# Performance work log

Measured on AMD Instinct MI355X. Metric: run time of the kernel, lower is better.

## Reference

```python
import jax, jax.numpy as jnp
import numpy as np
import math

B, S, D, H = 64, 575, 256, 8
FF = 4 * D
EPS = 1e-5
DILATIONS = (1, 2, 4)


def _ln(x, g, b):
    mu = jnp.mean(x, axis=-1, keepdims=True)
    var = jnp.var(x, axis=-1, keepdims=True)
    return (x - mu) * jax.lax.rsqrt(var + EPS) * g + b


def setup_inputs() -> dict:
    key = jax.random.key(0)
    ks = jax.random.split(key, 8)
    w = lambda k, shape: jax.random.normal(k, shape, jnp.float32) * 0.02
    return {
        'state': jax.random.normal(ks[0], (B, S, D), jnp.float32),
        'conv_w': w(ks[1], (3, D, D, 3, 3)),
        'conv_b': jnp.zeros((3, D), jnp.float32),
        'qkv_w': w(ks[2], (3 * D, D)),
        'qkv_b': jnp.zeros((3 * D,), jnp.float32),
        'o_w': w(ks[3], (D, D)),
        'o_b': jnp.zeros((D,), jnp.float32),
        'attn_bias': w(ks[4], (H, S, S)),
        'ffp_w': w(ks[5], (FF, D)),
        'ffp_b': jnp.zeros((FF,), jnp.float32),
        'ffg_w': w(ks[6], (FF, D)),
        'ffg_b': jnp.zeros((FF,), jnp.float32),
        'ffo_w': w(ks[7], (D, FF)),
        'ffo_b': jnp.zeros((D,), jnp.float32),
        'n1_g': jnp.ones((D,), jnp.float32), 'n1_b': jnp.zeros((D,), jnp.float32),
        'n2_g': jnp.ones((D,), jnp.float32), 'n2_b': jnp.zeros((D,), jnp.float32),
        'n3_g': jnp.ones((D,), jnp.float32), 'n3_b': jnp.zeros((D,), jnp.float32),
    }


def _forward(state, conv_w, conv_b, qkv_w, qkv_b, o_w, o_b, attn_bias,
             ffp_w, ffp_b, ffg_w, ffg_b, ffo_w, ffo_b,
             n1_g, n1_b, n2_g, n2_b, n3_g, n3_b):
    b, s, d = state.shape
    h = attn_bias.shape[0]
    hd = d // h
    spatial = int(round(math.sqrt(s + 1)))  # grid_size + 1; spatial^2 == s+1 here

    # --- multi-scale dilated conv mixing ---
    pad = jnp.zeros((b, 1, d), state.dtype)
    h2d = jnp.concatenate([pad, state], axis=1)            # (B, S+1, D)
    h2d = jnp.transpose(h2d, (0, 2, 1)).reshape(b, d, spatial, spatial)
    conv_sum = 0.0
    for i, dil in enumerate(DILATIONS):
        y = jax.lax.conv_general_dilated(
            h2d, conv_w[i], window_strides=(1, 1),
            padding=[(dil, dil), (dil, dil)], rhs_dilation=(dil, dil),
            dimension_numbers=('NCHW', 'OIHW', 'NCHW'))
        conv_sum = conv_sum + y + conv_b[i][None, :, None, None]
    h_flat = jnp.transpose(conv_sum.reshape(b, d, -1), (0, 2, 1))  # (B, S+1, D)
    hmix = h_flat[:, 1:, :]

    state = _ln(state + hmix, n1_g, n1_b)

    # --- self-attention with learned per-head pair bias ---
    qkv = state @ qkv_w.T + qkv_b                          # (B, S, 3D)
    q, k, v = jnp.split(qkv, 3, axis=-1)
    # NOTE: replicate torch's reshape (no transpose): (B,S,D) -> (B,H,S,hd)
    q = q.reshape(b, h, s, hd)
    k = k.reshape(b, h, s, hd)
    v = v.reshape(b, h, s, hd)
    scores = jnp.einsum('bhsd,bhtd->bhst', q, k) / math.sqrt(hd)
    scores = scores + attn_bias[None]
    attn = jax.nn.softmax(scores, axis=-1)
    out = jnp.einsum('bhst,bhtd->bhsd', attn, v)
    out = jnp.transpose(out, (0, 2, 1, 3)).reshape(b, s, d)

    state = _ln(state + out @ o_w.T + o_b, n2_g, n2_b)

    # --- gated feed-forward ---
    proj = state @ ffp_w.T + ffp_b
    gate = jax.nn.sigmoid(state @ ffg_w.T + ffg_b)
    ff = (proj * gate) @ ffo_w.T + ffo_b
    return _ln(state + ff, n3_g, n3_b)


def reference(state, conv_w, conv_b, qkv_w, qkv_b, o_w, o_b, attn_bias,
              ffp_w, ffp_b, ffg_w, ffg_b, ffo_w, ffo_b,
              n1_g, n1_b, n2_g, n2_b, n3_g, n3_b):
    return _forward(state, conv_w, conv_b, qkv_w, qkv_b, o_w, o_b, attn_bias,
                    ffp_w, ffp_b, ffg_w, ffg_b, ffo_w, ffo_b,
                    n1_g, n1_b, n2_g, n2_b, n3_g, n3_b)
```

## Files before the change

### kernel.cpp

```cpp
#include <hip/hip_runtime.h>
#include <hip/hip_bf16.h>
#include <cstdio>


typedef __attribute__((ext_vector_type(8))) short s8v;
typedef __attribute__((ext_vector_type(4))) float f32x4;
typedef unsigned short u16;

constexpr int kB = 64, kS = 575, kD = 256, kH = 8, kP = 576, kFF = 1024;
constexpr int kRows = kB * kS;
constexpr float kEps = 1e-5f;
constexpr float kScale = 0.17677669529663687f;
constexpr size_t kPdStride = 9420800;

__device__ __forceinline__ u16 f2b(float f) {
  __hip_bfloat16 h = __float2bfloat16(f);
  return *reinterpret_cast<u16*>(&h);
}
__device__ __forceinline__ void unpack2(unsigned int w, float& lo, float& hi) {
  union { float f; unsigned int u; } a, b;
  a.u = w << 16;
  b.u = w & 0xffff0000u;
  lo = a.f;
  hi = b.f;
}

__device__ __forceinline__ void gll16(const void* g, void* l) {
  __builtin_amdgcn_global_load_lds((const __attribute__((address_space(1))) void*)g,
                                   (__attribute__((address_space(3))) void*)l, 16, 0, 0);
}

__global__ void k_pack_convw(const float* __restrict__ cw, u16* __restrict__ wc) {
  const int blk = blockIdx.x;
  const int ci = threadIdx.x;
  const int i = blk >> 8, co = blk & 255;
  const float* src = cw + (size_t)blk * 2304 + ci * 9;
  float v[9];
#pragma unroll
  for (int r = 0; r < 9; ++r) v[r] = src[r];
#pragma unroll
  for (int r = 0; r < 9; ++r)
    wc[(((size_t)(i * 9 + r)) << 16) + (co << 8) + ci] = f2b(v[r]);
}

__global__ void k_tobf16(const float* __restrict__ in, u16* __restrict__ out, int n) {
  int i = blockIdx.x * 256 + threadIdx.x;
  if (i < n) out[i] = f2b(in[i]);
}

__global__ void k_make_x0(const float* __restrict__ state, u16* __restrict__ x0,
                          u16* __restrict__ zrow) {
  int bp = blockIdx.x;
  int c = threadIdx.x;
  if (bp == kB * kP) { zrow[c] = 0; return; }
  int p = bp % kP;
  int b = bp / kP;
  float v = (p == 0) ? 0.f : state[((size_t)(b * kS + p - 1)) * kD + c];
  x0[(size_t)bp * kD + c] = f2b(v);
}

__global__ __launch_bounds__(256) void k_gemm(const u16* __restrict__ A,
                                              const u16* __restrict__ Bw,
                                              const float* __restrict__ bias,
                                              u16* __restrict__ Cb,
                                              int M, int N, int K) {
  __shared__ u16 As[2][8192];
  __shared__ u16 Bs[2][8192];
  const int t = threadIdx.x;
  const int wave = t >> 6, lane = t & 63;
  const int wm = wave >> 1, wn = wave & 1;
  const int lr = lane & 15, lk = lane >> 4;
  const int m0 = blockIdx.x * 128, n0 = blockIdx.y * 128;
  const int lrow = lane >> 3;
  const int swzk = ((lane & 7) ^ lrow) * 8;
  const u16 *ga[4], *gb[4];
#pragma unroll
  for (int i = 0; i < 4; ++i) {
    int r = 8 * wave + lrow + 32 * i;
    int ra = m0 + r;
    if (ra > M - 1) ra = M - 1;
    ga[i] = A + (size_t)ra * K + swzk;
    gb[i] = Bw + (size_t)(n0 + r) * K + swzk;
  }
  auto stage = [&](int kt, int buf) {
#pragma unroll
    for (int i = 0; i < 4; ++i) {
      gll16(ga[i] + kt, &As[buf][i * 2048 + wave * 512]);
      gll16(gb[i] + kt, &Bs[buf][i * 2048 + wave * 512]);
    }
  };
  f32x4 acc[4][4] = {};
  stage(0, 0);
  __syncthreads();
  const int NT = K >> 6;
  for (int s = 0; s < NT; ++s) {
    const int cur = s & 1;
    if (s + 1 < NT) stage((s + 1) << 6, cur ^ 1);
    s8v af[2][4], bfr[2][4];
#pragma unroll
    for (int kk = 0; kk < 2; ++kk)
#pragma unroll
      for (int i = 0; i < 4; ++i) {
        const int rA = wm * 64 + i * 16 + lr;
        const int rB = wn * 64 + i * 16 + lr;
        af[kk][i] = *(const s8v*)(&As[cur][rA * 64 + ((kk * 32 + lk * 8) ^ ((rA & 7) << 3))]);
        bfr[kk][i] = *(const s8v*)(&Bs[cur][rB * 64 + ((kk * 32 + lk * 8) ^ ((rB & 7) << 3))]);
      }
#pragma unroll
    for (int kk = 0; kk < 2; ++kk)
#pragma unroll
      for (int i = 0; i < 4; ++i)
#pragma unroll
        for (int j = 0; j < 4; ++j)
          acc[i][j] = __builtin_amdgcn_mfma_f32_16x16x32_bf16(af[kk][i], bfr[kk][j], acc[i][j], 0, 0, 0);
    __syncthreads();
  }
#pragma unroll
  for (int i = 0; i < 4; ++i) {
    const int rbase = m0 + wm * 64 + i * 16 + lk * 4;
#pragma unroll
    for (int j = 0; j < 4; ++j) {
      const int col = n0 + wn * 64 + j * 16 + lr;
      const float bv = bias[col];
#pragma unroll
      for (int q = 0; q < 4; ++q) {
        int r = rbase + q;
        if (r < M) Cb[(size_t)r * N + col] = f2b(acc[i][j][q] + bv);
      }
    }
  }
}

__global__ __launch_bounds__(256) void k_ff1(const u16* __restrict__ A,
                                             const u16* __restrict__ Wf,
                                             const float* __restrict__ pb,
                                             const float* __restrict__ gb,
                                             u16* __restrict__ H, int M) {
  __shared__ u16 As[2][4096];
  __shared__ u16 Bp[2][4096];
  __shared__ u16 Bg[2][4096];
  const int t = threadIdx.x;
  const int wave = t >> 6;
  const int wm = wave >> 1, wn = wave & 1;
  const int lr = t & 15, lk = (t & 63) >> 4;
  const int m0 = blockIdx.x * 128, n0 = blockIdx.y * 128;
  int ra = m0 + (t >> 2);
  int rb = ra + 64;
  if (ra > M - 1) ra = M - 1;
  if (rb > M - 1) rb = M - 1;
  const int koff = (((t & 3) ^ ((t >> 2) & 3)) * 8);
  const u16* gA0 = A + (size_t)ra * kD + koff;
  const u16* gA1 = A + (size_t)rb * kD + koff;
  const u16* gP0 = Wf + (size_t)(n0 + (t >> 2)) * kD + koff;
  const u16* gP1 = gP0 + (size_t)64 * kD;
  const u16* gG0 = gP0 + (size_t)1024 * kD;
  const u16* gG1 = gP1 + (size_t)1024 * kD;
  auto stage = [&](int kt, int buf) {
    gll16(gA0 + kt, &As[buf][wave * 512]);
    gll16(gA1 + kt, &As[buf][2048 + wave * 512]);
    gll16(gP0 + kt, &Bp[buf][wave * 512]);
    gll16(gP1 + kt, &Bp[buf][2048 + wave * 512]);
    gll16(gG0 + kt, &Bg[buf][wave * 512]);
    gll16(gG1 + kt, &Bg[buf][2048 + wave * 512]);
  };
  f32x4 ap[4][4] = {};
  f32x4 ag[4][4] = {};
  stage(0, 0);
  __syncthreads();
  for (int s = 0; s < 8; ++s) {
    const int cur = s & 1;
    if (s < 7) stage((s + 1) << 5, cur ^ 1);
    s8v af[4], bp4[4], bg4[4];
#pragma unroll
    for (int i = 0; i < 4; ++i) {
      const int rA = wm * 64 + i * 16 + lr;
      const int rB = wn * 64 + i * 16 + lr;
      const int oA = rA * 32 + ((lk * 8) ^ ((rA & 3) << 3));
      const int oB = rB * 32 + ((lk * 8) ^ ((rB & 3) << 3));
      af[i] = *(const s8v*)(&As[cur][oA]);
      bp4[i] = *(const s8v*)(&Bp[cur][oB]);
      bg4[i] = *(const s8v*)(&Bg[cur][oB]);
    }
#pragma unroll
    for (int i = 0; i < 4; ++i)
#pragma unroll
      for (int j = 0; j < 4; ++j) {
        ap[i][j] = __builtin_amdgcn_mfma_f32_16x16x32_bf16(af[i], bp4[j], ap[i][j], 0, 0, 0);
        ag[i][j] = __builtin_amdgcn_mfma_f32_16x16x32_bf16(af[i], bg4[j], ag[i][j], 0, 0, 0);
      }
    __syncthreads();
  }
#pragma unroll
  for (int i = 0; i < 4; ++i) {
    const int rbase = m0 + wm * 64 + i * 16 + lk * 4;
#pragma unroll
    for (int j = 0; j < 4; ++j) {
      const int col = n0 + wn * 64 + j * 16 + lr;
      const float pbv = pb[col], gbv = gb[col];
#pragma unroll
      for (int q = 0; q < 4; ++q) {
        int r = rbase + q;
        if (r < M) {
          float p = ap[i][j][q] + pbv;
          float g = ag[i][j][q] + gbv;
          H[(size_t)r * kFF + col] = f2b(p * (1.f / (1.f + __expf(-g))));
        }
      }
    }
  }
}

__global__ __launch_bounds__(256) void k_conv(const u16* __restrict__ X0,
                                              const u16* __restrict__ zrow,
                                              const u16* __restrict__ Wc,
                                              const float* __restrict__ cb,
                                              u16* __restrict__ pd) {
  __shared__ u16 As[2][8192];
  __shared__ u16 Bs[2][8192];
  const int t = threadIdx.x;
  const int wave = t >> 6, lane = t & 63;
  const int wm = wave >> 1, wn = wave & 1;
  const int lr = lane & 15, lk = lane >> 4;
  const int m0 = blockIdx.x * 128;
  const int n0 = blockIdx.y * 128;
  const int di = blockIdx.z;
  const int dil = 1 << di;
  const int lrow = lane >> 3;
  const int swzk = ((lane & 7) ^ lrow) * 8;
  const u16* Wd = Wc + ((size_t)di * 9 << 16);
  int py[4], px[4];
  const u16* xrow[4];
  const u16* gw[4];
#pragma unroll
  for (int i = 0; i < 4; ++i) {
    int r = 8 * wave + lrow + 32 * i;
    int m = m0 + r;
    int bbv = m / 576;
    int p = m - bbv * 576;
    py[i] = p / 24;
    px[i] = p - py[i] * 24;
    xrow[i] = X0 + (((size_t)(bbv * kP)) << 8) + swzk;
    gw[i] = Wd + (size_t)(n0 + r) * kD + swzk;
  }
  const u16* S0[4];
  const u16* S1[4];
  auto csrc = [&](const u16** dst, int dyv, int dxv) {
#pragma unroll
    for (int i = 0; i < 4; ++i) {
      const int ny = py[i] + dyv, nx = px[i] + dxv;
      const bool v = ((unsigned)ny < 24u) & ((unsigned)nx < 24u);
      dst[i] = v ? xrow[i] + ((ny * 24 + nx) << 8) : zrow + swzk;
    }
  };
  auto stage = [&](const u16* const* S, size_t woff, int kc, int buf) {
#pragma unroll
    for (int i = 0; i < 4; ++i) {
      gll16(S[i] + kc, &As[buf][i * 2048 + wave * 512]);
      gll16(gw[i] + woff + kc, &Bs[buf][i * 2048 + wave * 512]);
    }
  };
  f32x4 acc[4][4] = {};
  csrc(S0, -dil, -dil);
  stage(S0, 0, 0, 0);
  stage(S0, 0, 64, 1);
  for (int tap = 0; tap < 9; ++tap) {
    if (tap < 8) {
      const int tn = tap + 1;
      csrc(S1, (tn / 3 - 1) * dil, (tn % 3 - 1) * dil);
    }
    const size_t woff = (size_t)tap << 16;
#pragma unroll
    for (int c = 0; c < 4; ++c) {
      const int buf = c & 1;
      if (c == 3 && tap == 8) {
        asm volatile("s_waitcnt vmcnt(0)" ::: "memory");
      } else {
        asm volatile("s_waitcnt vmcnt(8)" ::: "memory");
      }
      __builtin_amdgcn_s_barrier();
      s8v af[2][4], bfr[2][4];
#pragma unroll
      for (int kk = 0; kk < 2; ++kk)
#pragma unroll
        for (int ii = 0; ii < 4; ++ii) {
          const int rA = wm * 64 + ii * 16 + lr;
          const int rB = wn * 64 + ii * 16 + lr;
          af[kk][ii] = *(const s8v*)(&As[buf][rA * 64 + ((kk * 32 + lk * 8) ^ ((rA & 7) << 3))]);
          bfr[kk][ii] = *(const s8v*)(&Bs[buf][rB * 64 + ((kk * 32 + lk * 8) ^ ((rB & 7) << 3))]);
        }
#pragma unroll
      for (int kk = 0; kk < 2; ++kk)
#pragma unroll
        for (int ii = 0; ii < 4; ++ii)
#pragma unroll
          for (int jj = 0; jj < 4; ++jj)
            acc[ii][jj] = __builtin_amdgcn_mfma_f32_16x16x32_bf16(af[kk][ii], bfr[kk][jj], acc[ii][jj], 0, 0, 0);
      __builtin_amdgcn_s_barrier();
      if (c == 0) {
        stage(S0, woff, 128, buf);
      } else if (c == 1) {
        stage(S0, woff, 192, buf);
      } else if (c == 2) {
        if (tap < 8) stage(S1, woff + 65536, 0, buf);
      } else {
        if (tap < 8) stage(S1, woff + 65536, 64, buf);
      }
    }
#pragma unroll
    for (int i = 0; i < 4; ++i) S0[i] = S1[i];
  }
  u16* pdo = pd + (size_t)di * kPdStride;
#pragma unroll
  for (int i2 = 0; i2 < 4; ++i2) {
    const int mbase = m0 + wm * 64 + i2 * 16 + lk * 4;
#pragma unroll
    for (int j = 0; j < 4; ++j) {
      const int col = n0 + wn * 64 + j * 16 + lr;
      const float bv = cb[di * kD + col];
#pragma unroll
      for (int q = 0; q < 4; ++q) {
        const int m = mbase + q;
        const int b2 = m / 576;
        const int p = m - b2 * 576;
        if (p >= 1)
          pdo[((size_t)(b2 * kS + p - 1) << 8) + col] = f2b(acc[i2][j][q] + bv);
      }
    }
  }
}

__global__ __launch_bounds__(256) void k_attn2(const u16* __restrict__ qkv,
                                               const float* __restrict__ bias,
                                               u16* __restrict__ outp) {
  __shared__ u16 KsS[2][2048];
  __shared__ u16 VtS[2][2048];
  __shared__ u16 PsS[4][1024];
  const int qt = blockIdx.x, h = blockIdx.y, b = blockIdx.z;
  const int tid = threadIdx.x;
  const int w = tid >> 6, lane = tid & 63;
  const int lg = lane >> 4, lr = lane & 15;
  const int q0 = qt * 64;
  const int qrow_a = q0 + w * 16 + lr;
  const int qrow_ac = qrow_a < kS ? qrow_a : kS - 1;
  s8v qf;
  {
    int F = h * (kS * 32) + qrow_ac * 32 + lg * 8;
    qf = *(const s8v*)(qkv + ((size_t)(b * kS + (F >> 8))) * 768 + (F & 255));
  }
  const int trel = tid >> 2;
  const int dcol = (tid & 3) * 8;
  float mrun[4], lsum[4];
#pragma unroll
  for (int r = 0; r < 4; ++r) { mrun[r] = -1e30f; lsum[r] = 0.f; }
  f32x4 o0 = {0.f, 0.f, 0.f, 0.f}, o1 = {0.f, 0.f, 0.f, 0.f};
  const f32x4 zf = {0.f, 0.f, 0.f, 0.f};
  const int qrow_s = q0 + w * 16 + lg * 4;
  const size_t kvrowbase = (size_t)(b * kS) * 768;

  for (int kt = 0; kt < 9; ++kt) {
    const int t0 = kt * 64;
    const int buf = kt & 1;
    {
      const int tg = t0 + trel;
      const bool tv = tg < kS;
      const int tcl = tv ? tg : kS - 1;
      const int Fk = h * (kS * 32) + tcl * 32 + dcol;
      const u16* kp = qkv + kvrowbase + (size_t)(Fk >> 8) * 768 + 256 + (Fk & 255);
      uint4 kd = {0, 0, 0, 0}, vd = {0, 0, 0, 0};
      if (tv) {
        kd = *(const uint4*)kp;
        vd = *(const uint4*)(kp + 256);
      }
      *(uint4*)&KsS[buf][trel * 32 + (dcol ^ ((trel & 3) << 3))] = kd;
      union { uint4 u4; u16 us[8]; } vu;
      vu.u4 = vd;
#pragma unroll
      for (int j = 0; j < 8; ++j) {
        const int d = dcol + j;
        VtS[buf][d * 64 + (trel ^ ((d & 7) << 3))] = vu.us[j];
      }
    }
    float bv[4][4];
#pragma unroll
    for (int r = 0; r < 4; ++r) {
      const int qr = qrow_s + r;
      const float* bp = bias + ((size_t)h * kS + (qr < kS ? qr : kS - 1)) * kS;
#pragma unroll
      for (int j = 0; j < 4; ++j) {
        const int tg = t0 + j * 16 + lr;
        bv[j][r] = (tg < kS) ? bp[tg] : -1e30f;
      }
    }
    __syncthreads();
    f32x4 sc[4];
#pragma unroll
    for (int j = 0; j < 4; ++j) {
      const int krow = j * 16 + lr;
      s8v kf = *(const s8v*)&KsS[buf][krow * 32 + ((lg * 8) ^ ((krow & 3) << 3))];
      sc[j] = __builtin_amdgcn_mfma_f32_16x16x32_bf16(qf, kf, zf, 0, 0, 0);
    }
#pragma unroll
    for (int r = 0; r < 4; ++r) {
      float s4[4];
      float sm = -1e30f;
#pragma unroll
      for (int j = 0; j < 4; ++j) {
        s4[j] = fmaf(sc[j][r], kScale, bv[j][r]);
        sm = fmaxf(sm, s4[j]);
      }
      sm = fmaxf(sm, __shfl_xor(sm, 1));
      sm = fmaxf(sm, __shfl_xor(sm, 2));
      sm = fmaxf(sm, __shfl_xor(sm, 4));
      sm = fmaxf(sm, __shfl_xor(sm, 8));
      const float nm = fmaxf(mrun[r], sm);
      const float corr = __expf(mrun[r] - nm);
      mrun[r] = nm;
      float psum = 0.f;
      const int prow = lg * 4 + r;
#pragma unroll
      for (int j = 0; j < 4; ++j) {
        const float p = __expf(s4[j] - nm);
        psum += p;
        PsS[w][prow * 64 + ((j * 16 + lr) ^ ((prow & 7) << 3))] = f2b(p);
      }
      lsum[r] = fmaf(lsum[r], corr, psum);
      o0[r] *= corr;
      o1[r] *= corr;
    }
#pragma unroll
    for (int c = 0; c < 2; ++c) {
      const int pcol = c * 32 + lg * 8;
      s8v pf = *(const s8v*)&PsS[w][lr * 64 + (pcol ^ ((lr & 7) << 3))];
      s8v vf0 = *(const s8v*)&VtS[buf][lr * 64 + (pcol ^ ((lr & 7) << 3))];
      s8v vf1 = *(const s8v*)&VtS[buf][(16 + lr) * 64 + (pcol ^ (((16 + lr) & 7) << 3))];
      o0 = __builtin_amdgcn_mfma_f32_16x16x32_bf16(pf, vf0, o0, 0, 0, 0);
      o1 = __builtin_amdgcn_mfma_f32_16x16x32_bf16(pf, vf1, o1, 0, 0, 0);
    }
  }
#pragma unroll
  for (int r = 0; r < 4; ++r) {
    float lt = lsum[r];
    lt += __shfl_xor(lt, 1);
    lt += __shfl_xor(lt, 2);
    lt += __shfl_xor(lt, 4);
    lt += __shfl_xor(lt, 8);
    const float inv = 1.f / lt;
    const int qr = qrow_s + r;
    if (qr < kS) {
      u16* op = outp + ((size_t)(b * kS + qr)) * kD + h * 32;
      op[lr] = f2b(o0[r] * inv);
      op[16 + lr] = f2b(o1[r] * inv);
    }
  }
}

__global__ __launch_bounds__(256) void k_add_ln(const float* __restrict__ xa,
                                                const u16* __restrict__ xb,
                                                const float* __restrict__ g,
                                                const float* __restrict__ be,
                                                float* __restrict__ of, u16* __restrict__ ob) {
  const int wave = threadIdx.x >> 6, lane = threadIdx.x & 63;
  const int row = blockIdx.x * 4 + wave;
  const float4 a = ((const float4*)(xa + (size_t)row * kD))[lane];
  uint2 bw = ((const uint2*)(xb + (size_t)row * kD))[lane];
  float b0, b1, b2, b3;
  unpack2(bw.x, b0, b1);
  unpack2(bw.y, b2, b3);
  float x0 = a.x + b0, x1 = a.y + b1, x2 = a.z + b2, x3 = a.w + b3;
  float sum = x0 + x1 + x2 + x3;
  float sq = fmaf(x0, x0, fmaf(x1, x1, fmaf(x2, x2, x3 * x3)));
  for (int off = 1; off < 64; off <<= 1) {
    sum += __shfl_xor(sum, off);
    sq += __shfl_xor(sq, off);
  }
  const float mean = sum * (1.f / 256.f);
  const float var = sq * (1.f / 256.f) - mean * mean;
  const float rs = rsqrtf(var + kEps);
  const float4 gg = ((const float4*)g)[lane];
  const float4 bt = ((const float4*)be)[lane];
  float y0 = (x0 - mean) * rs * gg.x + bt.x;
  float y1 = (x1 - mean) * rs * gg.y + bt.y;
  float y2 = (x2 - mean) * rs * gg.z + bt.z;
  float y3 = (x3 - mean) * rs * gg.w + bt.w;
  float4 yo = {y0, y1, y2, y3};
  ((float4*)(of + (size_t)row * kD))[lane] = yo;
  if (ob) {
    u16* po = ob + (size_t)row * kD + lane * 4;
    po[0] = f2b(y0); po[1] = f2b(y1); po[2] = f2b(y2); po[3] = f2b(y3);
  }
}

__global__ __launch_bounds__(256) void k_add_ln3(const float* __restrict__ xa,
                                                 const u16* __restrict__ pa,
                                                 const u16* __restrict__ pbq,
                                                 const u16* __restrict__ pc,
                                                 const float* __restrict__ g,
                                                 const float* __restrict__ be,
                                                 float* __restrict__ of, u16* __restrict__ ob) {
  const int wave = threadIdx.x >> 6, lane = threadIdx.x & 63;
  const int row = blockIdx.x * 4 + wave;
  const size_t base = (size_t)row * kD;
  const float4 a = ((const float4*)(xa + base))[lane];
  uint2 w0 = ((const uint2*)(pa + base))[lane];
  uint2 w1 = ((const uint2*)(pbq + base))[lane];
  uint2 w2 = ((const uint2*)(pc + base))[lane];
  float a0, a1, a2, a3, c0, c1, c2, c3, d0, d1, d2, d3;
  unpack2(w0.x, a0, a1); unpack2(w0.y, a2, a3);
  unpack2(w1.x, c0, c1); unpack2(w1.y, c2, c3);
  unpack2(w2.x, d0, d1); unpack2(w2.y, d2, d3);
  float x0 = a.x + a0 + c0 + d0, x1 = a.y + a1 + c1 + d1;
  float x2 = a.z + a2 + c2 + d2, x3 = a.w + a3 + c3 + d3;
  float sum = x0 + x1 + x2 + x3;
  float sq = fmaf(x0, x0, fmaf(x1, x1, fmaf(x2, x2, x3 * x3)));
  for (int off = 1; off < 64; off <<= 1) {
    sum += __shfl_xor(sum, off);
    sq += __shfl_xor(sq, off);
  }
  const float mean = sum * (1.f / 256.f);
  const float var = sq * (1.f / 256.f) - mean * mean;
  const float rs = rsqrtf(var + kEps);
  const float4 gg = ((const float4*)g)[lane];
  const float4 bt = ((const float4*)be)[lane];
  float y0 = (x0 - mean) * rs * gg.x + bt.x;
  float y1 = (x1 - mean) * rs * gg.y + bt.y;
  float y2 = (x2 - mean) * rs * gg.z + bt.z;
  float y3 = (x3 - mean) * rs * gg.w + bt.w;
  float4 yo = {y0, y1, y2, y3};
  ((float4*)(of + base))[lane] = yo;
  u16* po = ob + base + lane * 4;
  po[0] = f2b(y0); po[1] = f2b(y1); po[2] = f2b(y2); po[3] = f2b(y3);
}

extern "C" void kernel_launch(void* const* d_in, const int* in_sizes, int n_in,
                              void* d_out, int out_size, void* d_ws, size_t ws_size,
                              hipStream_t stream) {
  const float* state = (const float*)d_in[0];
  const float* conv_w = (const float*)d_in[1];
  const float* conv_b = (const float*)d_in[2];
  const float* qkv_w = (const float*)d_in[3];
  const float* qkv_b = (const float*)d_in[4];
  const float* o_w = (const float*)d_in[5];
  const float* o_b = (const float*)d_in[6];
  const float* attn_bias = (const float*)d_in[7];
  const float* ffp_w = (const float*)d_in[8];
  const float* ffp_b = (const float*)d_in[9];
  const float* ffg_w = (const float*)d_in[10];
  const float* ffg_b = (const float*)d_in[11];
  const float* ffo_w = (const float*)d_in[12];
  const float* ffo_b = (const float*)d_in[13];
  const float* n1_g = (const float*)d_in[14];
  const float* n1_b = (const float*)d_in[15];
  const float* n2_g = (const float*)d_in[16];
  const float* n2_b = (const float*)d_in[17];
  const float* n3_g = (const float*)d_in[18];
  const float* n3_b = (const float*)d_in[19];

  constexpr size_t kWsNeed = 137527296;
  if (ws_size < kWsNeed) {
    fprintf(stderr, "[kernel] ws_size=%zu < need=%zu\n", ws_size, kWsNeed);
    return;
  }
  char* ws = (char*)d_ws;
  u16* Wc = (u16*)(ws + 0);
  u16* Wqkv = (u16*)(ws + 3538944);
  u16* Wo = (u16*)(ws + 3932160);
  u16* Wff = (u16*)(ws + 4063232);
  u16* Wffo = (u16*)(ws + 5111808);
  float* stF = (float*)(ws + 5636096);
  u16* stB = (u16*)(ws + 43319296);
  char* S4 = ws + 62160896;
  u16* X0 = (u16*)(ws + 5636096);
  u16* zrow = (u16*)(ws + 43319296);
  u16* pd = (u16*)S4;
  u16* qkvb = (u16*)S4;
  u16* attnout = (u16*)(S4 + 56524800);
  u16* oprojb = (u16*)S4;
  u16* ffh = (u16*)S4;
  float* outp = (float*)d_out;

  k_pack_convw<<<768, 256, 0, stream>>>(conv_w, Wc);
  k_tobf16<<<768, 256, 0, stream>>>(qkv_w, Wqkv, 768 * 256);
  k_tobf16<<<256, 256, 0, stream>>>(o_w, Wo, 256 * 256);
  k_tobf16<<<1024, 256, 0, stream>>>(ffp_w, Wff, 1024 * 256);
  k_tobf16<<<1024, 256, 0, stream>>>(ffg_w, Wff + 1024 * 256, 1024 * 256);
  k_tobf16<<<1024, 256, 0, stream>>>(ffo_w, Wffo, 256 * 1024);
  k_make_x0<<<kB * kP + 1, 256, 0, stream>>>(state, X0, zrow);

  k_conv<<<dim3(288, 2, 3), 256, 0, stream>>>(X0, zrow, Wc, conv_b, pd);
  k_add_ln3<<<kRows / 4, 256, 0, stream>>>(state, pd, pd + kPdStride, pd + 2 * kPdStride,
                                           n1_g, n1_b, stF, stB);

  k_gemm<<<dim3(288, 6), 256, 0, stream>>>(stB, Wqkv, qkv_b, qkvb, kRows, 768, 256);
  k_attn2<<<dim3(9, kH, kB), 256, 0, stream>>>(qkvb, attn_bias, attnout);
  k_gemm<<<dim3(288, 2), 256, 0, stream>>>(attnout, Wo, o_b, oprojb, kRows, 256, 256);
  k_add_ln<<<kRows / 4, 256, 0, stream>>>(stF, oprojb, n2_g, n2_b, stF, stB);

  k_ff1<<<dim3(288, 8), 256, 0, stream>>>(stB, Wff, ffp_b, ffg_b, ffh, kRows);
  k_gemm<<<dim3(288, 2), 256, 0, stream>>>(ffh, Wffo, ffo_b, stB, kRows, 256, 1024);
  k_add_ln<<<kRows / 4, 256, 0, stream>>>(stF, stB, n3_g, n3_b, outp, nullptr);
}
```

Baseline: 516.9 us.

## Make GEMMs persistent over multiple M tiles with cross-tile prefetch pipeline

Each GEMM block now processes several consecutive 128-row M tiles, flattening tile and K iterations into one loop. The next stage's loads are issued across tile boundaries, so the prologue and epilogue latency of each tile is hidden. Explicit vmcnt waits and raw barriers replace __syncthreads to keep two stages in flight. The trade-off is fewer blocks, which lowers occupancy and parallelism; the hand-counted vmcnt values depend on the exact number of loads issued per stage.

```diff
diff --git a/kernel.cpp b/kernel.cpp
--- a/kernel.cpp
+++ b/kernel.cpp
@@ -63,39 +63,48 @@
                                               const u16* __restrict__ Bw,
                                               const float* __restrict__ bias,
                                               u16* __restrict__ Cb,
-                                              int M, int N, int K) {
+                                              int M, int N, int K, int MT, int ntSh) {
   __shared__ u16 As[2][8192];
   __shared__ u16 Bs[2][8192];
   const int t = threadIdx.x;
   const int wave = t >> 6, lane = t & 63;
   const int wm = wave >> 1, wn = wave & 1;
   const int lr = lane & 15, lk = lane >> 4;
-  const int m0 = blockIdx.x * 128, n0 = blockIdx.y * 128;
+  const int n0 = blockIdx.y * 128;
   const int lrow = lane >> 3;
   const int swzk = ((lane & 7) ^ lrow) * 8;
-  const u16 *ga[4], *gb[4];
+  int roff[4];
+  const u16* gb[4];
 #pragma unroll
   for (int i = 0; i < 4; ++i) {
     int r = 8 * wave + lrow + 32 * i;
-    int ra = m0 + r;
-    if (ra > M - 1) ra = M - 1;
-    ga[i] = A + (size_t)ra * K + swzk;
+    roff[i] = r;
     gb[i] = Bw + (size_t)(n0 + r) * K + swzk;
   }
-  auto stage = [&](int kt, int buf) {
+  const int NT = 1 << ntSh;
+  const int U = MT << ntSh;
+  auto stage = [&](int u, int buf) {
+    const int mt = u >> ntSh;
+    const int kt = (u & (NT - 1)) << 6;
+    const int m0 = (blockIdx.x * MT + mt) << 7;
 #pragma unroll
     for (int i = 0; i < 4; ++i) {
-      gll16(ga[i] + kt, &As[buf][i * 2048 + wave * 512]);
+      int ra = m0 + roff[i];
+      if (ra > M - 1) ra = M - 1;
+      gll16(A + (size_t)ra * K + kt + swzk, &As[buf][i * 2048 + wave * 512]);
       gll16(gb[i] + kt, &Bs[buf][i * 2048 + wave * 512]);
     }
   };
   f32x4 acc[4][4] = {};
   stage(0, 0);
-  __syncthreads();
-  const int NT = K >> 6;
-  for (int s = 0; s < NT; ++s) {
-    const int cur = s & 1;
-    if (s + 1 < NT) stage((s + 1) << 6, cur ^ 1);
+  if (U > 1) stage(1, 1);
+  for (int u = 0; u < U; ++u) {
+    const int cur = u & 1;
+    if (u + 1 < U)
+      asm volatile("s_waitcnt vmcnt(8)" ::: "memory");
+    else
+      asm volatile("s_waitcnt vmcnt(0)" ::: "memory");
+    __builtin_amdgcn_s_barrier();
     s8v af[2][4], bfr[2][4];
 #pragma unroll
     for (int kk = 0; kk < 2; ++kk)
@@ -113,19 +122,24 @@
 #pragma unroll
         for (int j = 0; j < 4; ++j)
           acc[i][j] = __builtin_amdgcn_mfma_f32_16x16x32_bf16(af[kk][i], bfr[kk][j], acc[i][j], 0, 0, 0);
-    __syncthreads();
-  }
-#pragma unroll
-  for (int i = 0; i < 4; ++i) {
-    const int rbase = m0 + wm * 64 + i * 16 + lk * 4;
-#pragma unroll
-    for (int j = 0; j < 4; ++j) {
-      const int col = n0 + wn * 64 + j * 16 + lr;
-      const float bv = bias[col];
-#pragma unroll
-      for (int q = 0; q < 4; ++q) {
-        int r = rbase + q;
-        if (r < M) Cb[(size_t)r * N + col] = f2b(acc[i][j][q] + bv);
+    __builtin_amdgcn_s_barrier();
+    if (u + 2 < U) stage(u + 2, cur);
+    if ((u & (NT - 1)) == NT - 1) {
+      const int m0 = (blockIdx.x * MT + (u >> ntSh)) << 7;
+#pragma unroll
+      for (int i = 0; i < 4; ++i) {
+        const int rbase = m0 + wm * 64 + i * 16 + lk * 4;
+#pragma unroll
+        for (int j = 0; j < 4; ++j) {
+          const int col = n0 + wn * 64 + j * 16 + lr;
+          const float bv = bias[col];
+#pragma unroll
+          for (int q = 0; q < 4; ++q) {
+            int r = rbase + q;
+            if (r < M) Cb[(size_t)r * N + col] = f2b(acc[i][j][q] + bv);
+          }
+          acc[i][j] = (f32x4){0.f, 0.f, 0.f, 0.f};
+        }
       }
     }
   }
@@ -135,7 +149,7 @@
                                              const u16* __restrict__ Wf,
                                              const float* __restrict__ pb,
                                              const float* __restrict__ gb,
-                                             u16* __restrict__ H, int M) {
+                                             u16* __restrict__ H, int M, int MT) {
   __shared__ u16 As[2][4096];
   __shared__ u16 Bp[2][4096];
   __shared__ u16 Bg[2][4096];
@@ -143,21 +157,24 @@
   const int wave = t >> 6;
   const int wm = wave >> 1, wn = wave & 1;
   const int lr = t & 15, lk = (t & 63) >> 4;
-  const int m0 = blockIdx.x * 128, n0 = blockIdx.y * 128;
-  int ra = m0 + (t >> 2);
-  int rb = ra + 64;
-  if (ra > M - 1) ra = M - 1;
-  if (rb > M - 1) rb = M - 1;
+  const int n0 = blockIdx.y * 128;
   const int koff = (((t & 3) ^ ((t >> 2) & 3)) * 8);
-  const u16* gA0 = A + (size_t)ra * kD + koff;
-  const u16* gA1 = A + (size_t)rb * kD + koff;
-  const u16* gP0 = Wf + (size_t)(n0 + (t >> 2)) * kD + koff;
+  const int r0 = t >> 2;
+  const u16* gP0 = Wf + (size_t)(n0 + r0) * kD + koff;
   const u16* gP1 = gP0 + (size_t)64 * kD;
   const u16* gG0 = gP0 + (size_t)1024 * kD;
   const u16* gG1 = gP1 + (size_t)1024 * kD;
-  auto stage = [&](int kt, int buf) {
-    gll16(gA0 + kt, &As[buf][wave * 512]);
-    gll16(gA1 + kt, &As[buf][2048 + wave * 512]);
+  const int U = MT << 3;
+  auto stage = [&](int u, int buf) {
+    const int mt = u >> 3;
+    const int kt = (u & 7) << 5;
+    const int m0 = (blockIdx.x * MT + mt) << 7;
+    int ra = m0 + r0;
+    int rb = ra + 64;
+    if (ra > M - 1) ra = M - 1;
+    if (rb > M - 1) rb = M - 1;
+    gll16(A + (size_t)ra * kD + kt + koff, &As[buf][wave * 512]);
+    gll16(A + (size_t)rb * kD + kt + koff, &As[buf][2048 + wave * 512]);
     gll16(gP0 + kt, &Bp[buf][wave * 512]);
     gll16(gP1 + kt, &Bp[buf][2048 + wave * 512]);
     gll16(gG0 + kt, &Bg[buf][wave * 512]);
@@ -166,10 +183,14 @@
   f32x4 ap[4][4] = {};
   f32x4 ag[4][4] = {};
   stage(0, 0);
-  __syncthreads();
-  for (int s = 0; s < 8; ++s) {
-    const int cur = s & 1;
-    if (s < 7) stage((s + 1) << 5, cur ^ 1);
+  if (U > 1) stage(1, 1);
+  for (int u = 0; u < U; ++u) {
+    const int cur = u & 1;
+    if (u + 1 < U)
+      asm volatile("s_waitcnt vmcnt(6)" ::: "memory");
+    else
+      asm volatile("s_waitcnt vmcnt(0)" ::: "memory");
+    __builtin_amdgcn_s_barrier();
     s8v af[4], bp4[4], bg4[4];
 #pragma unroll
     for (int i = 0; i < 4; ++i) {
@@ -188,22 +209,28 @@
         ap[i][j] = __builtin_amdgcn_mfma_f32_16x16x32_bf16(af[i], bp4[j], ap[i][j], 0, 0, 0);
         ag[i][j] = __builtin_amdgcn_mfma_f32_16x16x32_bf16(af[i], bg4[j], ag[i][j], 0, 0, 0);
       }
-    __syncthreads();
-  }
-#pragma unroll
-  for (int i = 0; i < 4; ++i) {
-    const int rbase = m0 + wm * 64 + i * 16 + lk * 4;
-#pragma unroll
-    for (int j = 0; j < 4; ++j) {
-      const int col = n0 + wn * 64 + j * 16 + lr;
-      const float pbv = pb[col], gbv = gb[col];
-#pragma unroll
-      for (int q = 0; q < 4; ++q) {
-        int r = rbase + q;
-        if (r < M) {
-          float p = ap[i][j][q] + pbv;
-          float g = ag[i][j][q] + gbv;
-          H[(size_t)r * kFF + col] = f2b(p * (1.f / (1.f + __expf(-g))));
+    __builtin_amdgcn_s_barrier();
+    if (u + 2 < U) stage(u + 2, cur);
+    if ((u & 7) == 7) {
+      const int m0 = (blockIdx.x * MT + (u >> 3)) << 7;
+#pragma unroll
+      for (int i = 0; i < 4; ++i) {
+        const int rbase = m0 + wm * 64 + i * 16 + lk * 4;
+#pragma unroll
+        for (int j = 0; j < 4; ++j) {
+          const int col = n0 + wn * 64 + j * 16 + lr;
+          const float pbv = pb[col], gbv = gb[col];
+#pragma unroll
+          for (int q = 0; q < 4; ++q) {
+            int r = rbase + q;
+            if (r < M) {
+              float p = ap[i][j][q] + pbv;
+              float g = ag[i][j][q] + gbv;
+              H[(size_t)r * kFF + col] = f2b(p * (1.f / (1.f + __expf(-g))));
+            }
+          }
+          ap[i][j] = (f32x4){0.f, 0.f, 0.f, 0.f};
+          ag[i][j] = (f32x4){0.f, 0.f, 0.f, 0.f};
         }
       }
     }
@@ -590,12 +617,12 @@
   k_add_ln3<<<kRows / 4, 256, 0, stream>>>(state, pd, pd + kPdStride, pd + 2 * kPdStride,
                                            n1_g, n1_b, stF, stB);
 
-  k_gemm<<<dim3(288, 6), 256, 0, stream>>>(stB, Wqkv, qkv_b, qkvb, kRows, 768, 256);
+  k_gemm<<<dim3(72, 6), 256, 0, stream>>>(stB, Wqkv, qkv_b, qkvb, kRows, 768, 256, 4, 2);
   k_attn2<<<dim3(9, kH, kB), 256, 0, stream>>>(qkvb, attn_bias, attnout);
-  k_gemm<<<dim3(288, 2), 256, 0, stream>>>(attnout, Wo, o_b, oprojb, kRows, 256, 256);
+  k_gemm<<<dim3(144, 2), 256, 0, stream>>>(attnout, Wo, o_b, oprojb, kRows, 256, 256, 2, 2);
   k_add_ln<<<kRows / 4, 256, 0, stream>>>(stF, oprojb, n2_g, n2_b, stF, stB);
 
-  k_ff1<<<dim3(288, 8), 256, 0, stream>>>(stB, Wff, ffp_b, ffg_b, ffh, kRows);
-  k_gemm<<<dim3(288, 2), 256, 0, stream>>>(ffh, Wffo, ffo_b, stB, kRows, 256, 1024);
+  k_ff1<<<dim3(144, 8), 256, 0, stream>>>(stB, Wff, ffp_b, ffg_b, ffh, kRows, 2);
+  k_gemm<<<dim3(144, 2), 256, 0, stream>>>(ffh, Wffo, ffo_b, stB, kRows, 256, 1024, 2, 4);
   k_add_ln<<<kRows / 4, 256, 0, stream>>>(stF, stB, n3_g, n3_b, outp, nullptr);
 }
```

Result: slower. 690.8 us (+33.6%).
